# Kernel optimization log

Hardware: AMD Instinct MI355X
Metric: run time of the kernel (lower is better)

The kernel has to match this reference:

```python
import jax, jax.numpy as jnp
import numpy as np

WINDOW_SIZES = (1, 2, 3)
COV_DIM = 128
MEM_DIM = 128
BATCH = 8192


def setup_inputs() -> dict:
    rng = np.random.default_rng(0)
    sizes = rng.integers(16, 64, size=BATCH)
    total = int(sizes.sum())  # ~327k tokens
    key = jax.random.key(0)
    ks = jax.random.split(key, 10)
    s = 0.05
    inp = {
        "x": jax.random.normal(ks[0], (total, COV_DIM), jnp.float32),
        "sizes": jnp.asarray(sizes, jnp.int32),
    }
    for i, w in enumerate(WINDOW_SIZES):
        inp[f"conv_w{i}"] = jax.random.normal(ks[1 + 2 * i], (MEM_DIM, COV_DIM, w), jnp.float32) * s
        inp[f"conv_b{i}"] = jax.random.normal(ks[2 + 2 * i], (MEM_DIM,), jnp.float32) * s
    inp["lin_w"] = jax.random.normal(ks[7], (MEM_DIM, len(WINDOW_SIZES) * MEM_DIM), jnp.float32) * s
    inp["lin_b"] = jax.random.normal(ks[8], (MEM_DIM,), jnp.float32) * s
    return inp


def _temporal_conv(x, w, b):
    # x: [T, C], w: [M, C, k] -> [T-k+1, M]  (valid 1D conv, as nn.Conv1d)
    y = jax.lax.conv_general_dilated(
        x.T[None],  # [1, C, T]
        w,
        window_strides=(1,),
        padding="VALID",
        dimension_numbers=("NCH", "OIH", "NCH"),
    )[0]  # [M, L]
    return y.T + b


def _dmax(h, sizes, window_size, batch):
    # Ragged per-segment max over dim 0 of the concatenated conv output.
    # Segment i covers rows [off_i, off_i + sizes[i] - window_size + 1) where
    # off_i is the exclusive cumsum of sizes (DMax advances start_idx by sizes[i]).
    L = h.shape[0]  # total - window_size + 1
    cum = jnp.cumsum(sizes)  # [B], inclusive
    p = jnp.arange(L)
    seg = jnp.searchsorted(cum, p, side="right")  # segment owning row p
    valid = p + (window_size - 1) < cum[seg]  # within sizes[i]-w+1 prefix
    seg = jnp.where(valid, seg, batch)  # dump invalid rows in a trash segment
    return jax.ops.segment_max(h, seg, num_segments=batch + 1)[:batch]


def reference(x, sizes, conv_w0, conv_b0, conv_w1, conv_b1, conv_w2, conv_b2, lin_w, lin_b):
    batch = sizes.shape[0]
    convs = ((conv_w0, conv_b0), (conv_w1, conv_b1), (conv_w2, conv_b2))
    pools = []
    for wsz, (cw, cb) in zip(WINDOW_SIZES, convs):
        h = jax.nn.relu(_temporal_conv(x, cw, cb))  # [T-w+1, M]
        pools.append(_dmax(h, sizes, wsz, batch))  # [B, M]
    concat = jnp.concatenate(pools, axis=1)  # [B, 3M]
    return jnp.tanh(concat @ lin_w.T + lin_b)  # [B, M]
```

## Files before the change

kernel.cpp:

```cpp
#include <hip/hip_runtime.h>
#include <hip/hip_bf16.h>

typedef __bf16 bf16x8 __attribute__((ext_vector_type(8)));
typedef __bf16 bf16x4 __attribute__((ext_vector_type(4)));
typedef float  f32x4  __attribute__((ext_vector_type(4)));

#define MFMA16(a, b, c) __builtin_amdgcn_mfma_f32_16x16x32_bf16((a), (b), (c), 0, 0, 0)

__global__ void k_prep(const int* __restrict__ sizes, int* __restrict__ offsets,
                       const float* __restrict__ w0, const float* __restrict__ w1,
                       const float* __restrict__ w2, const float* __restrict__ lw,
                       __bf16* __restrict__ Wpack,
                       __bf16* __restrict__ Lhi, __bf16* __restrict__ Llo) {
  const int bid = blockIdx.x, t = threadIdx.x;
  if (bid == 240) {
    __shared__ int part[256];
    const int base = t * 32;
    int v[32];
    int s = 0;
#pragma unroll
    for (int i = 0; i < 32; ++i) { v[i] = sizes[base + i]; s += v[i]; }
    part[t] = s;
    __syncthreads();
    for (int d = 1; d < 256; d <<= 1) {
      int add = (t >= d) ? part[t - d] : 0;
      __syncthreads();
      part[t] += add;
      __syncthreads();
    }
    int run = (t == 0) ? 0 : part[t - 1];
#pragma unroll
    for (int i = 0; i < 32; ++i) { offsets[base + i] = run; run += v[i]; }
  } else if (bid < 48) {
    const int nt = bid, sl = nt >> 3, f = nt & 7;
    const int kt = t >> 6, lane = t & 63;
    const float* src; int kw, jj;
    if      (sl == 0) { src = w0; kw = 1; jj = 0; }
    else if (sl == 1) { src = w1; kw = 2; jj = 0; }
    else if (sl == 2) { src = w1; kw = 2; jj = 1; }
    else if (sl == 3) { src = w2; kw = 3; jj = 0; }
    else if (sl == 4) { src = w2; kw = 3; jj = 1; }
    else              { src = w2; kw = 3; jj = 2; }
    const int feat  = f * 16 + (lane & 15);
    const int cbase = kt * 32 + ((lane >> 4) << 3);
    __bf16* dst = Wpack + ((((nt * 4 + kt) << 6) + lane) << 3);
#pragma unroll
    for (int j = 0; j < 8; ++j)
      dst[j] = (__bf16)src[(feat * 128 + cbase + j) * kw + jj];
  } else {
    const int idx = (bid - 48) * 256 + t;
    const int j = idx & 7, lane = (idx >> 3) & 63, rest = idx >> 9;
    const int kt = rest % 12, nt = rest / 12;
    const int o = nt * 16 + (lane & 15);
    const int q = kt * 32 + ((lane >> 4) << 3) + j;
    const float v = lw[o * 384 + q];
    const __bf16 hi = (__bf16)v;
    Lhi[idx] = hi;
    Llo[idx] = (__bf16)(v - (float)hi);
  }
}

#define SPB 32

__global__ __launch_bounds__(512, 2)
void k_conv(const float* __restrict__ x, const int* __restrict__ sizes,
            const int* __restrict__ offsets,
            const float* __restrict__ cb0, const float* __restrict__ cb1,
            const float* __restrict__ cb2,
            const bf16x8* __restrict__ Wpack,
            __bf16* __restrict__ Phi, __bf16* __restrict__ Plo) {
  __shared__ __align__(16) __bf16 xs[2][66 * 128];
  const int t = threadIdx.x;
  const int wid = t >> 6, lane = t & 63;
  const int lo16 = lane & 15, g16 = lane >> 4;

  bf16x8 wf[6][4];
#pragma unroll
  for (int sl = 0; sl < 6; ++sl)
#pragma unroll
    for (int kt = 0; kt < 4; ++kt)
      wf[sl][kt] = Wpack[(((sl * 8 + wid) * 4 + kt) << 6) + lane];

  const int xr0 = lo16 & 7, xr1 = (lo16 + 1) & 7, xr2 = (lo16 + 2) & 7;
  const int seg0 = blockIdx.x * SPB;

  int s_cur = sizes[seg0];
  const long o_cur = offsets[seg0];

  {
    const int uend = (((s_cur + 15) >> 4) * 16 + 2) << 4;
#pragma unroll
    for (int k = 0; k < 3; ++k) {
      const int u = t + (k << 9);
      if (u < uend) {
        const int r = u >> 4, g = u & 15;
        bf16x8 h;
        if (r < s_cur) {
          const float* p = x + (o_cur + r) * 128 + (g << 3);
          const float4 a = *(const float4*)p;
          const float4 b = *(const float4*)(p + 4);
          h[0] = (__bf16)a.x; h[1] = (__bf16)a.y; h[2] = (__bf16)a.z; h[3] = (__bf16)a.w;
          h[4] = (__bf16)b.x; h[5] = (__bf16)b.y; h[6] = (__bf16)b.z; h[7] = (__bf16)b.w;
        } else {
#pragma unroll
          for (int j = 0; j < 8; ++j) h[j] = (__bf16)0.f;
        }
        *(bf16x8*)&xs[0][r * 128 + ((g ^ (r & 7)) << 3)] = h;
      }
    }
  }
  __syncthreads();

  int cur = 0;
  int s_nn = sizes[seg0 + 1];
  int o_nn = offsets[seg0 + 1];

  for (int i = 0; i < SPB; ++i) {
    const int seg = seg0 + i;
    const int s = s_cur;
    const int MT = (s + 15) >> 4;

    const int s_nxt = s_nn;
    const long o_nxt = o_nn;
    float4 va[3], vb[3];
    bool act[3] = {false, false, false}, lv[3] = {false, false, false};
    if (i + 1 < SPB) {
      const int uend = (((s_nxt + 15) >> 4) * 16 + 2) << 4;
#pragma unroll
      for (int k = 0; k < 3; ++k) {
        const int u = t + (k << 9);
        const int r = u >> 4, g = u & 15;
        act[k] = (u < uend);
        lv[k] = act[k] && (r < s_nxt);
        if (lv[k]) {
          const float* p = x + (o_nxt + r) * 128 + (g << 3);
          va[k] = *(const float4*)p;
          vb[k] = *(const float4*)(p + 4);
        }
      }
      if (i + 2 < SPB) {
        s_nn = sizes[seg0 + i + 2];
        o_nn = offsets[seg0 + i + 2];
      }
    }

    f32x4 acc[4][3];
#pragma unroll
    for (int mt = 0; mt < 4; ++mt)
#pragma unroll
      for (int p = 0; p < 3; ++p)
        acc[mt][p] = f32x4{0.f, 0.f, 0.f, 0.f};

    const __bf16* xb = xs[cur];
#pragma unroll
    for (int kt = 0; kt < 4; ++kt) {
      const int gg = kt * 4 + g16;
#pragma unroll
      for (int mt = 0; mt < 4; ++mt) {
        if (mt < MT) {
          const int rb = mt * 16 + lo16;
          const bf16x8 A0 = *(const bf16x8*)&xb[(rb    ) * 128 + ((gg ^ xr0) << 3)];
          const bf16x8 A1 = *(const bf16x8*)&xb[(rb + 1) * 128 + ((gg ^ xr1) << 3)];
          const bf16x8 A2 = *(const bf16x8*)&xb[(rb + 2) * 128 + ((gg ^ xr2) << 3)];
          acc[mt][0] = MFMA16(A0, wf[0][kt], acc[mt][0]);
          acc[mt][1] = MFMA16(A0, wf[1][kt], acc[mt][1]);
          acc[mt][2] = MFMA16(A0, wf[3][kt], acc[mt][2]);
          acc[mt][1] = MFMA16(A1, wf[2][kt], acc[mt][1]);
          acc[mt][2] = MFMA16(A1, wf[4][kt], acc[mt][2]);
          acc[mt][2] = MFMA16(A2, wf[5][kt], acc[mt][2]);
        }
      }
    }

    if (i + 1 < SPB) {
#pragma unroll
      for (int k = 0; k < 3; ++k) {
        if (act[k]) {
          const int u = t + (k << 9);
          const int r = u >> 4, g = u & 15;
          bf16x8 h;
          if (lv[k]) {
            h[0] = (__bf16)va[k].x; h[1] = (__bf16)va[k].y;
            h[2] = (__bf16)va[k].z; h[3] = (__bf16)va[k].w;
            h[4] = (__bf16)vb[k].x; h[5] = (__bf16)vb[k].y;
            h[6] = (__bf16)vb[k].z; h[7] = (__bf16)vb[k].w;
          } else {
#pragma unroll
            for (int j = 0; j < 8; ++j) h[j] = (__bf16)0.f;
          }
          *(bf16x8*)&xs[cur ^ 1][r * 128 + ((g ^ (r & 7)) << 3)] = h;
        }
      }
    }

    float m1 = -3e38f, m2 = -3e38f, m3 = -3e38f;
#pragma unroll
    for (int mt = 0; mt < 4; ++mt) {
      if (mt < MT) {
#pragma unroll
        for (int v = 0; v < 4; ++v) {
          const int lrow = mt * 16 + g16 * 4 + v;
          if (lrow < s)     m1 = fmaxf(m1, acc[mt][0][v]);
          if (lrow < s - 1) m2 = fmaxf(m2, acc[mt][1][v]);
          if (lrow < s - 2) m3 = fmaxf(m3, acc[mt][2][v]);
        }
      }
    }
    m1 = fmaxf(m1, __shfl_xor(m1, 16)); m1 = fmaxf(m1, __shfl_xor(m1, 32));
    m2 = fmaxf(m2, __shfl_xor(m2, 16)); m2 = fmaxf(m2, __shfl_xor(m2, 32));
    m3 = fmaxf(m3, __shfl_xor(m3, 16)); m3 = fmaxf(m3, __shfl_xor(m3, 32));
    if (g16 == 0) {
      const int feat = wid * 16 + lo16;
      const float p1 = fmaxf(m1 + cb0[feat], 0.f);
      const float p2 = fmaxf(m2 + cb1[feat], 0.f);
      const float p3 = fmaxf(m3 + cb2[feat], 0.f);
      const __bf16 h1 = (__bf16)p1, h2 = (__bf16)p2, h3 = (__bf16)p3;
      const long row = (long)seg * 384;
      Phi[row + feat]       = h1;
      Plo[row + feat]       = (__bf16)(p1 - (float)h1);
      Phi[row + 128 + feat] = h2;
      Plo[row + 128 + feat] = (__bf16)(p2 - (float)h2);
      Phi[row + 256 + feat] = h3;
      Plo[row + 256 + feat] = (__bf16)(p3 - (float)h3);
    }

    __syncthreads();
    s_cur = s_nxt;
    cur ^= 1;
  }
}

__global__ __launch_bounds__(256, 4)
void k_lin(const __bf16* __restrict__ Phi, const __bf16* __restrict__ Plo,
           const bf16x8* __restrict__ Lhi, const bf16x8* __restrict__ Llo,
           const float* __restrict__ lb, float* __restrict__ out) {
  __shared__ __bf16 ph[16 * 392];
  __shared__ __bf16 pl[16 * 392];
  const int blk = blockIdx.x, t = threadIdx.x;
  const long rbase = (long)blk * 16;
#pragma unroll
  for (int i = 0; i < 3; ++i) {
    const int ci = t + (i << 8);
    const int r = ci / 48, cc = ci % 48;
    *(int4*)&ph[r * 392 + (cc << 3)] = *(const int4*)&Phi[(rbase + r) * 384 + (cc << 3)];
    *(int4*)&pl[r * 392 + (cc << 3)] = *(const int4*)&Plo[(rbase + r) * 384 + (cc << 3)];
  }
  __syncthreads();
  const int wid = t >> 6, lane = t & 63;
  const int lo16 = lane & 15, g = lane >> 4;
#pragma unroll
  for (int ni = 0; ni < 2; ++ni) {
    const int nt = wid + (ni << 2);
    f32x4 acc = f32x4{0.f, 0.f, 0.f, 0.f};
#pragma unroll
    for (int kt = 0; kt < 12; ++kt) {
      const bf16x8 bh = Lhi[((nt * 12 + kt) << 6) + lane];
      const bf16x8 bl = Llo[((nt * 12 + kt) << 6) + lane];
      const int aoff = lo16 * 392 + kt * 32 + (g << 3);
      const bf16x8 ah = *(const bf16x8*)&ph[aoff];
      const bf16x8 al = *(const bf16x8*)&pl[aoff];
      acc = MFMA16(ah, bh, acc);
      acc = MFMA16(al, bh, acc);
      acc = MFMA16(ah, bl, acc);
    }
    const int o = nt * 16 + lo16;
    const float bias = lb[o];
#pragma unroll
    for (int v = 0; v < 4; ++v) {
      const int r = g * 4 + v;
      const float val = acc[v] + bias;
      out[(rbase + r) * 128 + o] = 1.f - 2.f / (__expf(2.f * val) + 1.f);
    }
  }
}

extern "C" void kernel_launch(void* const* d_in, const int* in_sizes, int n_in,
                              void* d_out, int out_size, void* d_ws, size_t ws_size,
                              hipStream_t stream) {
  const float* x   = (const float*)d_in[0];
  const int* sizes = (const int*)d_in[1];
  const float* w0  = (const float*)d_in[2];
  const float* cb0 = (const float*)d_in[3];
  const float* w1  = (const float*)d_in[4];
  const float* cb1 = (const float*)d_in[5];
  const float* w2  = (const float*)d_in[6];
  const float* cb2 = (const float*)d_in[7];
  const float* lw  = (const float*)d_in[8];
  const float* lb  = (const float*)d_in[9];

  char* ws = (char*)d_ws;
  size_t o = 0;
  int*    offsets = (int*)ws;                 o += 32768;
  __bf16* Wpack   = (__bf16*)(ws + o);        o += 196608;
  __bf16* Lhi     = (__bf16*)(ws + o);        o += 98304;
  __bf16* Llo     = (__bf16*)(ws + o);        o += 98304;
  __bf16* Phi     = (__bf16*)(ws + o);        o += 8192L * 384 * 2;
  __bf16* Plo     = (__bf16*)(ws + o);        o += 8192L * 384 * 2;

  k_prep<<<241, 256, 0, stream>>>(sizes, offsets, w0, w1, w2, lw, Wpack, Lhi, Llo);
  k_conv<<<256, 512, 0, stream>>>(x, sizes, offsets, cb0, cb1, cb2,
                                  (const bf16x8*)Wpack, Phi, Plo);
  k_lin<<<512, 256, 0, stream>>>(Phi, Plo, (const bf16x8*)Lhi,
                                 (const bf16x8*)Llo, lb, (float*)d_out);
}
```

Baseline: 331.0 us.

## Stream conv weights per k-tile and halve segments per block for occupancy

The conv kernel no longer keeps all 24 weight fragments resident in registers. It reloads the six B fragments for each k-tile from global/L2 inside the MFMA loop, and the launch bound rises to four blocks per CU. Segments per block drop from 32 to 16, which doubles the grid to 512 blocks so more waves per CU can hide load latency. Tail rows are no longer zero-filled in shared memory, relying on the row masks in the max reduction. The cost is repeated weight fetches for every segment, and stale LDS rows now feed MFMAs whose outputs are masked out.

Result: slower. 696.8 us (+110.5%).

```diff
diff --git a/kernel.cpp b/kernel.cpp
--- a/kernel.cpp
+++ b/kernel.cpp
@@ -60,9 +60,9 @@
   }
 }
 
-#define SPB 32
-
-__global__ __launch_bounds__(512, 2)
+#define SPB 16
+
+__global__ __launch_bounds__(512, 4)
 void k_conv(const float* __restrict__ x, const int* __restrict__ sizes,
             const int* __restrict__ offsets,
             const float* __restrict__ cb0, const float* __restrict__ cb1,
@@ -73,38 +73,24 @@
   const int t = threadIdx.x;
   const int wid = t >> 6, lane = t & 63;
   const int lo16 = lane & 15, g16 = lane >> 4;
-
-  bf16x8 wf[6][4];
-#pragma unroll
-  for (int sl = 0; sl < 6; ++sl)
-#pragma unroll
-    for (int kt = 0; kt < 4; ++kt)
-      wf[sl][kt] = Wpack[(((sl * 8 + wid) * 4 + kt) << 6) + lane];
-
   const int xr0 = lo16 & 7, xr1 = (lo16 + 1) & 7, xr2 = (lo16 + 2) & 7;
   const int seg0 = blockIdx.x * SPB;
 
   int s_cur = sizes[seg0];
-  const long o_cur = offsets[seg0];
-
   {
-    const int uend = (((s_cur + 15) >> 4) * 16 + 2) << 4;
-#pragma unroll
-    for (int k = 0; k < 3; ++k) {
+    const long o_cur = offsets[seg0];
+    const int uend = s_cur << 4;
+#pragma unroll
+    for (int k = 0; k < 2; ++k) {
       const int u = t + (k << 9);
       if (u < uend) {
         const int r = u >> 4, g = u & 15;
+        const float* p = x + (o_cur + r) * 128 + (g << 3);
+        const float4 a = *(const float4*)p;
+        const float4 b = *(const float4*)(p + 4);
         bf16x8 h;
-        if (r < s_cur) {
-          const float* p = x + (o_cur + r) * 128 + (g << 3);
-          const float4 a = *(const float4*)p;
-          const float4 b = *(const float4*)(p + 4);
-          h[0] = (__bf16)a.x; h[1] = (__bf16)a.y; h[2] = (__bf16)a.z; h[3] = (__bf16)a.w;
-          h[4] = (__bf16)b.x; h[5] = (__bf16)b.y; h[6] = (__bf16)b.z; h[7] = (__bf16)b.w;
-        } else {
-#pragma unroll
-          for (int j = 0; j < 8; ++j) h[j] = (__bf16)0.f;
-        }
+        h[0] = (__bf16)a.x; h[1] = (__bf16)a.y; h[2] = (__bf16)a.z; h[3] = (__bf16)a.w;
+        h[4] = (__bf16)b.x; h[5] = (__bf16)b.y; h[6] = (__bf16)b.z; h[7] = (__bf16)b.w;
         *(bf16x8*)&xs[0][r * 128 + ((g ^ (r & 7)) << 3)] = h;
       }
     }
@@ -121,27 +107,29 @@
     const int MT = (s + 15) >> 4;
 
     const int s_nxt = s_nn;
-    const long o_nxt = o_nn;
-    float4 va[3], vb[3];
-    bool act[3] = {false, false, false}, lv[3] = {false, false, false};
+    const long o_nxt = (long)o_nn;
+    float4 va0, vb0, va1, vb1;
+    bool a0 = false, a1 = false;
     if (i + 1 < SPB) {
-      const int uend = (((s_nxt + 15) >> 4) * 16 + 2) << 4;
-#pragma unroll
-      for (int k = 0; k < 3; ++k) {
-        const int u = t + (k << 9);
-        const int r = u >> 4, g = u & 15;
-        act[k] = (u < uend);
-        lv[k] = act[k] && (r < s_nxt);
-        if (lv[k]) {
+      const int uend = s_nxt << 4;
+      {
+        a0 = t < uend;
+        if (a0) {
+          const int r = t >> 4, g = t & 15;
           const float* p = x + (o_nxt + r) * 128 + (g << 3);
-          va[k] = *(const float4*)p;
-          vb[k] = *(const float4*)(p + 4);
-        }
-      }
-      if (i + 2 < SPB) {
-        s_nn = sizes[seg0 + i + 2];
-        o_nn = offsets[seg0 + i + 2];
-      }
+          va0 = *(const float4*)p; vb0 = *(const float4*)(p + 4);
+        }
+      }
+      {
+        const int u = t + 512;
+        a1 = u < uend;
+        if (a1) {
+          const int r = u >> 4, g = u & 15;
+          const float* p = x + (o_nxt + r) * 128 + (g << 3);
+          va1 = *(const float4*)p; vb1 = *(const float4*)(p + 4);
+        }
+      }
+      if (i + 2 < SPB) { s_nn = sizes[seg + 2]; o_nn = offsets[seg + 2]; }
     }
 
     f32x4 acc[4][3];
@@ -154,42 +142,44 @@
     const __bf16* xb = xs[cur];
 #pragma unroll
     for (int kt = 0; kt < 4; ++kt) {
+      bf16x8 bf[6];
+#pragma unroll
+      for (int sl = 0; sl < 6; ++sl)
+        bf[sl] = Wpack[(((sl * 8 + wid) * 4 + kt) << 6) + lane];
       const int gg = kt * 4 + g16;
+      const int c0 = (gg ^ xr0) << 3, c1 = (gg ^ xr1) << 3, c2 = (gg ^ xr2) << 3;
 #pragma unroll
       for (int mt = 0; mt < 4; ++mt) {
         if (mt < MT) {
-          const int rb = mt * 16 + lo16;
-          const bf16x8 A0 = *(const bf16x8*)&xb[(rb    ) * 128 + ((gg ^ xr0) << 3)];
-          const bf16x8 A1 = *(const bf16x8*)&xb[(rb + 1) * 128 + ((gg ^ xr1) << 3)];
-          const bf16x8 A2 = *(const bf16x8*)&xb[(rb + 2) * 128 + ((gg ^ xr2) << 3)];
-          acc[mt][0] = MFMA16(A0, wf[0][kt], acc[mt][0]);
-          acc[mt][1] = MFMA16(A0, wf[1][kt], acc[mt][1]);
-          acc[mt][2] = MFMA16(A0, wf[3][kt], acc[mt][2]);
-          acc[mt][1] = MFMA16(A1, wf[2][kt], acc[mt][1]);
-          acc[mt][2] = MFMA16(A1, wf[4][kt], acc[mt][2]);
-          acc[mt][2] = MFMA16(A2, wf[5][kt], acc[mt][2]);
+          const int rb = (mt * 16 + lo16) * 128;
+          const bf16x8 A0 = *(const bf16x8*)&xb[rb + c0];
+          const bf16x8 A1 = *(const bf16x8*)&xb[rb + 128 + c1];
+          const bf16x8 A2 = *(const bf16x8*)&xb[rb + 256 + c2];
+          acc[mt][0] = MFMA16(A0, bf[0], acc[mt][0]);
+          acc[mt][1] = MFMA16(A0, bf[1], acc[mt][1]);
+          acc[mt][2] = MFMA16(A0, bf[3], acc[mt][2]);
+          acc[mt][1] = MFMA16(A1, bf[2], acc[mt][1]);
+          acc[mt][2] = MFMA16(A1, bf[4], acc[mt][2]);
+          acc[mt][2] = MFMA16(A2, bf[5], acc[mt][2]);
         }
       }
     }
 
     if (i + 1 < SPB) {
-#pragma unroll
-      for (int k = 0; k < 3; ++k) {
-        if (act[k]) {
-          const int u = t + (k << 9);
-          const int r = u >> 4, g = u & 15;
-          bf16x8 h;
-          if (lv[k]) {
-            h[0] = (__bf16)va[k].x; h[1] = (__bf16)va[k].y;
-            h[2] = (__bf16)va[k].z; h[3] = (__bf16)va[k].w;
-            h[4] = (__bf16)vb[k].x; h[5] = (__bf16)vb[k].y;
-            h[6] = (__bf16)vb[k].z; h[7] = (__bf16)vb[k].w;
-          } else {
-#pragma unroll
-            for (int j = 0; j < 8; ++j) h[j] = (__bf16)0.f;
-          }
-          *(bf16x8*)&xs[cur ^ 1][r * 128 + ((g ^ (r & 7)) << 3)] = h;
-        }
+      if (a0) {
+        const int r = t >> 4, g = t & 15;
+        bf16x8 h;
+        h[0] = (__bf16)va0.x; h[1] = (__bf16)va0.y; h[2] = (__bf16)va0.z; h[3] = (__bf16)va0.w;
+        h[4] = (__bf16)vb0.x; h[5] = (__bf16)vb0.y; h[6] = (__bf16)vb0.z; h[7] = (__bf16)vb0.w;
+        *(bf16x8*)&xs[cur ^ 1][r * 128 + ((g ^ (r & 7)) << 3)] = h;
+      }
+      if (a1) {
+        const int u = t + 512;
+        const int r = u >> 4, g = u & 15;
+        bf16x8 h;
+        h[0] = (__bf16)va1.x; h[1] = (__bf16)va1.y; h[2] = (__bf16)va1.z; h[3] = (__bf16)va1.w;
+        h[4] = (__bf16)vb1.x; h[5] = (__bf16)vb1.y; h[6] = (__bf16)vb1.z; h[7] = (__bf16)vb1.w;
+        *(bf16x8*)&xs[cur ^ 1][r * 128 + ((g ^ (r & 7)) << 3)] = h;
       }
     }
 
@@ -298,7 +288,7 @@
   __bf16* Plo     = (__bf16*)(ws + o);        o += 8192L * 384 * 2;
 
   k_prep<<<241, 256, 0, stream>>>(sizes, offsets, w0, w1, w2, lw, Wpack, Lhi, Llo);
-  k_conv<<<256, 512, 0, stream>>>(x, sizes, offsets, cb0, cb1, cb2,
+  k_conv<<<512, 512, 0, stream>>>(x, sizes, offsets, cb0, cb1, cb2,
                                   (const bf16x8*)Wpack, Phi, Plo);
   k_lin<<<512, 256, 0, stream>>>(Phi, Plo, (const bf16x8*)Lhi,
                                  (const bf16x8*)Llo, lb, (float*)d_out);
```
